# Kernel optimization log

Hardware: AMD Instinct MI355X
Metric: run time of the kernel (lower is better)

The kernel has to match this reference:

```python
import jax, jax.numpy as jnp
import numpy as np
from jax import lax

NUM_MASK_PARAMS = 67  # 66 weights (64 feat + 2 coord channels) + 1 bias
NUM_GEN_PARAMS = 134


def _coord_maps(h, w, dtype):
    yy = jnp.broadcast_to(jnp.linspace(-1.0, 1.0, h, dtype=dtype)[:, None], (h, w))
    xx = jnp.broadcast_to(jnp.linspace(-1.0, 1.0, w, dtype=dtype)[None, :], (h, w))
    return xx, yy


def _dynamic_head(x_cat, p):
    # x_cat: [66, H, W]; p: [num_ins, 67] -> [num_ins, H, W]
    w = p[:, :NUM_MASK_PARAMS - 1]
    b = p[:, NUM_MASK_PARAMS - 1]
    return jnp.einsum('ic,chw->ihw', w, x_cat) + b[:, None, None]


def setup_inputs() -> dict:
    key = jax.random.key(0)
    ks = jax.random.split(key, 10)
    C, HM, WM, HH, WH, MB, HID = 256, 272, 480, 136, 240, 64, 64
    rn = lambda k, s, sc=1.0: jax.random.normal(k, s, dtype=jnp.float32) * sc
    return {
        'out0': rn(ks[0], (1, C, HM, WM)),
        'out1': rn(ks[1], (1, C, HH, WH)),
        'hm_w': rn(ks[2], (1, C), 0.05),
        'hm_b': jnp.zeros((1,), jnp.float32),
        'params_w': rn(ks[3], (NUM_GEN_PARAMS, C), 0.05),
        'params_b': rn(ks[4], (NUM_GEN_PARAMS,), 0.05),
        'mb_w': rn(ks[5], (MB, C, 3, 3), 0.05),
        'mb_b': jnp.zeros((MB,), jnp.float32),
        'mlp_w1': rn(ks[6], (HM, HID), 0.05),
        'mlp_b1': jnp.zeros((HID,), jnp.float32),
        'mlp_w2': rn(ks[7], (HID, 2), 0.05),
        'mlp_b2': jnp.zeros((2,), jnp.float32),
        'num_ins': 4,
    }


def reference(out0, out1, hm_w, hm_b, params_w, params_b, mb_w, mb_b,
              mlp_w1, mlp_b1, mlp_w2, mlp_b2, num_ins):
    h_mask, w_mask = out0.shape[2], out0.shape[3]
    h_hm, w_hm = out1.shape[2], out1.shape[3]

    # ctnet head: 1x1 convs on the stride-16 feature
    hm = jnp.einsum('kc,bchw->bkhw', hm_w, out1) + hm_b[None, :, None, None]
    params = jnp.einsum('kc,bchw->bkhw', params_w, out1) + params_b[None, :, None, None]
    hm = jnp.clip(jax.nn.sigmoid(hm), 1e-4, 1.0 - 1e-4)  # [1,1,h_hm,w_hm]
    # [1,134,h,w] -> [h*w, 134]
    params_flat = jnp.transpose(params[0], (1, 2, 0)).reshape(-1, NUM_GEN_PARAMS)

    # 3x3 maxpool NMS (stride 1, pad 1), keep only local peaks
    hmax = lax.reduce_window(hm, -jnp.inf, lax.max, (1, 1, 3, 3), (1, 1, 1, 1),
                             [(0, 0), (0, 0), (1, 1), (1, 1)])
    keep = (hmax == hm).astype(hm.dtype)
    heat_nms = (hm * keep).reshape(-1)

    scores, inds = lax.top_k(heat_nms, num_ins)

    # mask branch: 3x3 conv + relu on the stride-8 feature
    mask_branch = lax.conv_general_dilated(out0, mb_w, (1, 1), 'SAME',
                                           dimension_numbers=('NCHW', 'OIHW', 'NCHW'))
    mask_branch = jax.nn.relu(mask_branch + mb_b[None, :, None, None])  # [1,64,H,W]

    xx, yy = _coord_maps(h_mask, w_mask, mask_branch.dtype)
    x_cat = jnp.concatenate([mask_branch[0], xx[None], yy[None]], axis=0)  # [66,H,W]

    gen_params = params_flat[inds]  # [num_ins, 134]
    masks0 = _dynamic_head(x_cat, gen_params[:, :NUM_MASK_PARAMS])   # [num_ins,H,W]
    regs0 = _dynamic_head(x_cat, gen_params[:, NUM_MASK_PARAMS:])    # [num_ins,H,W]

    # row-wise vertical-range MLP over h_mask
    feat_range = jnp.transpose(masks0, (0, 2, 1))  # [num_ins, w_mask, h_mask]
    h1 = jax.nn.relu(feat_range @ mlp_w1 + mlp_b1)
    feat_range = h1 @ mlp_w2 + mlp_b2  # [num_ins, w_mask, 2]

    return scores, inds, regs0, masks0, feat_range
```

## Files before the change

kernel.cpp:

```cpp
#include <hip/hip_runtime.h>
#include <math.h>
#include <limits.h>

#define C_IN 256
#define HM_H 136
#define HM_W 240
#define HM_N (HM_H * HM_W)
#define MB   64
#define MH   272
#define MW   480
#define MN   (MH * MW)
#define NP   134
#define NI   4
#define HID  64

#define REG_OFF   8
#define MASK_OFF  (8 + NI * MN)
#define FEAT_OFF  (8 + 2 * NI * MN)

#define WS_HM   0
#define WS_CV   HM_N
#define WS_CI   (HM_N + 512)
#define WS_GP   (2 * HM_N)
#define WS_WT_F 65824

typedef float  f32x4  __attribute__((ext_vector_type(4)));
typedef short  bf16x8 __attribute__((ext_vector_type(8)));
typedef unsigned int u32x4 __attribute__((ext_vector_type(4)));

__device__ __forceinline__ unsigned short f2bf(float f) {
  unsigned int u = __float_as_uint(f);
  u += 0x7FFFu + ((u >> 16) & 1u);
  return (unsigned short)(u >> 16);
}
__device__ __forceinline__ float b2f(unsigned short h) {
  return __uint_as_float(((unsigned int)h) << 16);
}
__device__ __forceinline__ unsigned cvtpk(float a, float b) {
  unsigned r;
  asm("v_cvt_pk_bf16_f32 %0, %1, %2" : "=v"(r) : "v"(a), "v"(b));
  return r;
}

__device__ __forceinline__ void glds16(const void* g, void* l) {
  __builtin_amdgcn_global_load_lds(
      (const __attribute__((address_space(1))) unsigned int*)g,
      (__attribute__((address_space(3))) unsigned int*)l, 16, 0, 0);
}

__global__ void k_prep(const float* __restrict__ mb_w, unsigned short* __restrict__ wt,
                       const float* __restrict__ out1, const float* __restrict__ hm_w,
                       const float* __restrict__ hm_b, float* __restrict__ ws_hm) {
  __shared__ float part[4][64];
  if (blockIdx.x < 576) {
    int idx = blockIdx.x * 256 + threadIdx.x;
    int j    = idx & 7;
    int lane = (idx >> 3) & 63;
    int nt   = (idx >> 9) & 3;
    int gt   = idx >> 11;
    int t    = gt % 9;
    int g    = gt / 9;
    int n = nt * 16 + (lane & 15);
    int c = g * 32 + (lane >> 4) * 8 + j;
    wt[idx] = f2bf(mb_w[(n * C_IN + c) * 9 + t]);
  } else {
    int b = blockIdx.x - 576, t = threadIdx.x;
    int cg = t >> 6, pl = t & 63;
    int p = b * 64 + pl;
    float s = 0.f;
    #pragma unroll 16
    for (int c = 0; c < 64; ++c)
      s += hm_w[cg * 64 + c] * out1[(cg * 64 + c) * HM_N + p];
    part[cg][pl] = s;
    __syncthreads();
    if (t < 64) {
      float tot = part[0][t] + part[1][t] + part[2][t] + part[3][t] + hm_b[0];
      float sig = 1.f / (1.f + expf(-tot));
      sig = fminf(fmaxf(sig, 1e-4f), 1.f - 1e-4f);
      ws_hm[b * 64 + t] = sig;
    }
  }
}

__device__ __forceinline__ bool better(float av, int ai, float bv, int bi) {
  return (av > bv) || (av == bv && ai < bi);
}

template<int NTHR>
__device__ void top4_tree(float* sv, int* si, int t) {
  for (int s = NTHR / 2; s >= 1; s >>= 1) {
    if (t < s) {
      float a[4], b[4]; int ai[4], bj[4];
      #pragma unroll
      for (int k = 0; k < 4; ++k) {
        a[k] = sv[t * 4 + k];        ai[k] = si[t * 4 + k];
        b[k] = sv[(t + s) * 4 + k];  bj[k] = si[(t + s) * 4 + k];
      }
      float ov[4]; int oi[4];
      int i = 0, j = 0;
      #pragma unroll
      for (int k = 0; k < 4; ++k) {
        if (better(a[i], ai[i], b[j], bj[j])) { ov[k] = a[i]; oi[k] = ai[i]; ++i; }
        else                                   { ov[k] = b[j]; oi[k] = bj[j]; ++j; }
      }
      #pragma unroll
      for (int k = 0; k < 4; ++k) { sv[t * 4 + k] = ov[k]; si[t * 4 + k] = oi[k]; }
    }
    __syncthreads();
  }
}

__global__ void k_nms_top(const float* __restrict__ ws_hm, float* __restrict__ candv,
                          int* __restrict__ candi) {
  __shared__ float sv[256 * 4];
  __shared__ int   si[256 * 4];
  int b = blockIdx.x, t = threadIdx.x;
  float v = -1.f; int idx = INT_MAX;
  if (t < 255) {
    int p = b * 255 + t;
    int y = p / HM_W, x = p - y * HM_W;
    float c = ws_hm[p], m = c;
    #pragma unroll
    for (int dy = -1; dy <= 1; ++dy)
      #pragma unroll
      for (int dx = -1; dx <= 1; ++dx) {
        int yy = y + dy, xx = x + dx;
        if (yy >= 0 && yy < HM_H && xx >= 0 && xx < HM_W)
          m = fmaxf(m, ws_hm[yy * HM_W + xx]);
      }
    v = (c == m) ? c : 0.f;
    idx = p;
  }
  sv[t * 4] = v; si[t * 4] = idx;
  #pragma unroll
  for (int k = 1; k < 4; ++k) { sv[t * 4 + k] = -1.f; si[t * 4 + k] = INT_MAX; }
  __syncthreads();
  top4_tree<256>(sv, si, t);
  if (t == 0) {
    #pragma unroll
    for (int k = 0; k < 4; ++k) { candv[b * 4 + k] = sv[k]; candi[b * 4 + k] = si[k]; }
  }
}

__global__ void k_gen(const float* __restrict__ candv, const int* __restrict__ candi,
                      const float* __restrict__ out1, const float* __restrict__ params_w,
                      const float* __restrict__ params_b, float* __restrict__ ws_gp,
                      float* __restrict__ d_out) {
  __shared__ float sv[128 * 4];
  __shared__ int   si[128 * 4];
  __shared__ float col[C_IN];
  __shared__ float part[NP];
  int t = threadIdx.x, i = blockIdx.x;
  if (t < 128) {
    #pragma unroll
    for (int k = 0; k < 4; ++k) { sv[t * 4 + k] = candv[t * 4 + k]; si[t * 4 + k] = candi[t * 4 + k]; }
  }
  __syncthreads();
  top4_tree<128>(sv, si, t);
  if (i == 0 && t < 4) {
    d_out[t]     = sv[t];
    d_out[4 + t] = (float)si[t];
  }
  int p = si[i];
  if (t < 256) col[t] = out1[t * HM_N + p];
  __syncthreads();
  int half = t >> 8, jj = t & 255;
  float s = 0.f;
  if (jj < NP) {
    s = half ? 0.f : params_b[jj];
    const float* pw = params_w + jj * C_IN + half * 128;
    const float* cl = col + half * 128;
    #pragma unroll 8
    for (int c = 0; c < 128; ++c) s += pw[c] * cl[c];
    if (half) part[jj] = s;
  }
  __syncthreads();
  if (!half && jj < NP) ws_gp[i * NP + jj] = s + part[jj];
}

#define SR   18
#define RP   36
#define BUFU (SR * RP * 32)
#define WBASE (2 * BUFU)
#define WBUFU 18432

#define PIPE_BARRIER() do {                                   \
    __builtin_amdgcn_sched_barrier(0);                        \
    asm volatile("s_waitcnt lgkmcnt(0)" ::: "memory");        \
    __builtin_amdgcn_s_barrier();                             \
    __builtin_amdgcn_sched_barrier(0);                        \
  } while (0)

#define STAGE_W_ALL(G)                                                    \
  if (wv == 7 && (G) < 8) {                                               \
    const char* wsrc = (const char*)wt + (G) * 36864 + lane * 16;         \
    char* wdst = (char*)smem + 82944 + ((G) & 1) * 36864;                 \
    _Pragma("unroll")                                                     \
    for (int i_ = 0; i_ < 36; ++i_)                                       \
      glds16(wsrc + i_ * 1024, wdst + i_ * 1024);                         \
  }

#define MFMA16(A, B, C) __builtin_amdgcn_mfma_f32_16x16x32_bf16(A, B, C, 0, 0, 0)

#define TAPS3(P) {                                                        \
    const unsigned short* wl = smem + WBASE + ((g) & 1) * WBUFU           \
                               + (P) * 6144 + lane * 8;                   \
    _Pragma("unroll")                                                     \
    for (int tt = 0; tt < 3; ++tt) {                                      \
      bf16x8 bb0 = *(const bf16x8*)(wl + tt * 2048);                      \
      bf16x8 bb1 = *(const bf16x8*)(wl + tt * 2048 + 512);                \
      bf16x8 bb2 = *(const bf16x8*)(wl + tt * 2048 + 1024);               \
      bf16x8 bb3 = *(const bf16x8*)(wl + tt * 2048 + 1536);               \
      unsigned pk = lrdp[(P) * 3 + tt];                                   \
      const unsigned short* c0 = cur + (pk & 0xFFFFu);                    \
      const unsigned short* c1 = cur + (pk >> 16);                        \
      bf16x8 a0 = *(const bf16x8*)c0;                                     \
      bf16x8 a1 = *(const bf16x8*)(c0 + 512);                             \
      bf16x8 a2 = *(const bf16x8*)c1;                                     \
      bf16x8 a3 = *(const bf16x8*)(c1 + 512);                             \
      acc[0][0] = MFMA16(a0, bb0, acc[0][0]);                             \
      acc[0][1] = MFMA16(a0, bb1, acc[0][1]);                             \
      acc[0][2] = MFMA16(a0, bb2, acc[0][2]);                             \
      acc[0][3] = MFMA16(a0, bb3, acc[0][3]);                             \
      acc[1][0] = MFMA16(a1, bb0, acc[1][0]);                             \
      acc[1][1] = MFMA16(a1, bb1, acc[1][1]);                             \
      acc[1][2] = MFMA16(a1, bb2, acc[1][2]);                             \
      acc[1][3] = MFMA16(a1, bb3, acc[1][3]);                             \
      acc[2][0] = MFMA16(a2, bb0, acc[2][0]);                             \
      acc[2][1] = MFMA16(a2, bb1, acc[2][1]);                             \
      acc[2][2] = MFMA16(a2, bb2, acc[2][2]);                             \
      acc[2][3] = MFMA16(a2, bb3, acc[2][3]);                             \
      acc[3][0] = MFMA16(a3, bb0, acc[3][0]);                             \
      acc[3][1] = MFMA16(a3, bb1, acc[3][1]);                             \
      acc[3][2] = MFMA16(a3, bb2, acc[3][2]);                             \
      acc[3][3] = MFMA16(a3, bb3, acc[3][3]);                             \
    } }

__device__ __forceinline__ void stage_store8(unsigned short* buf, const f32x4* dq,
                                             const int* lw, unsigned sm) {
  #pragma unroll
  for (int e = 0; e < 4; ++e) if ((sm >> e) & 1u) {
    u32x4 v;
    v[0] = cvtpk(dq[0][e], dq[1][e]);
    v[1] = cvtpk(dq[2][e], dq[3][e]);
    v[2] = cvtpk(dq[4][e], dq[5][e]);
    v[3] = cvtpk(dq[6][e], dq[7][e]);
    *(u32x4*)(buf + lw[e]) = v;
  }
}

__global__ __launch_bounds__(512, 2) void k_conv_mfma(
    const float* __restrict__ out0, const unsigned short* __restrict__ wt,
    const float* __restrict__ mb_b, const float* __restrict__ ws_gp,
    float* __restrict__ d_out) {
  __shared__ unsigned short smem[2 * BUFU + 2 * WBUFU];

  int tid  = threadIdx.x;
  int lane = tid & 63;
  int wv   = tid >> 6;
  int n15  = lane & 15;
  int kq   = lane >> 4;

  int orig = blockIdx.x;
  int xcd  = orig & 7, pos = orig >> 3;
  int wgid = (xcd < 7) ? (xcd * 32 + pos) : (224 + pos);
  int bx = wgid / 17, by = wgid - bx * 17;
  int gx0 = bx * 32, gy0 = by * 16;

  bool ustage = tid < 360;
  int u    = ustage ? tid : 0;
  int co8  = u / 180;
  int rem  = u - co8 * 180;
  int row  = rem / 10;
  int qx   = rem - row * 10;
  int iy   = gy0 + row - 1;
  int ixq  = gx0 + 4 * qx - 4;
  bool gvld = ustage && (iy >= 0) && (iy < MH) && (ixq >= 0) && (ixq + 3 < MW);
  int goffA = gvld ? (co8 * 8 * MN + iy * MW + ixq) : 0;
  int lwsA[4]; unsigned smask = 0;
  #pragma unroll
  for (int e = 0; e < 4; ++e) {
    int sx = 4 * qx - 3 + e;
    bool sv = ustage && (sx >= 0) && (sx < RP);
    int pixw = row * RP + (sv ? sx : 0);
    int w2 = (pixw ^ (pixw >> 2)) & 3;
    int q  = (pixw ^ row) & 1;
    lwsA[e] = (pixw >> 1) * 64 + ((co8 ^ w2) << 4) + q * 8;
    if (sv) smask |= (1u << e);
  }

  unsigned lrdp[9];
  #pragma unroll
  for (int t = 0; t < 9; ++t) {
    int ty = t / 3, tx = t - ty * 3;
    int sr0 = 2 * wv + ty;
    int pix0 = sr0 * RP + n15 + tx;
    int w20 = (pix0 ^ (pix0 >> 2)) & 3;
    int q0  = (pix0 ^ sr0) & 1;
    unsigned o0 = (pix0 >> 1) * 64 + ((kq ^ w20) << 4) + q0 * 8;
    int sr1 = sr0 + 1;
    int pix1 = sr1 * RP + n15 + tx;
    int w21 = (pix1 ^ (pix1 >> 2)) & 3;
    int q1  = (pix1 ^ sr1) & 1;
    unsigned o1 = (pix1 >> 1) * 64 + ((kq ^ w21) << 4) + q1 * 8;
    lrdp[t] = o0 | (o1 << 16);
  }

  f32x4 dqA[8], dqB[8];
  #pragma unroll
  for (int j = 0; j < 8; ++j) {
    dqA[j] = (f32x4){0.f, 0.f, 0.f, 0.f};
    dqB[j] = (f32x4){0.f, 0.f, 0.f, 0.f};
  }
  if (gvld) {
    const float* sp = out0 + goffA;
    #pragma unroll
    for (int j = 0; j < 8; ++j) dqA[j] = *(const f32x4*)(sp + j * MN);
  }
  stage_store8(smem, dqA, lwsA, smask);
  if (gvld) {
    const float* sp = out0 + goffA + 16 * MN;
    #pragma unroll
    for (int j = 0; j < 8; ++j) dqB[j] = *(const f32x4*)(sp + j * MN);
  }
  {
    int lwsB[4];
    #pragma unroll
    for (int e = 0; e < 4; ++e) lwsB[e] = lwsA[e] ^ 32;
    stage_store8(smem, dqB, lwsB, smask);
  }
  __builtin_amdgcn_sched_barrier(0);
  if (gvld) {
    const float* sp = out0 + 32 * MN + goffA;
    #pragma unroll
    for (int j = 0; j < 8; ++j) dqA[j] = *(const f32x4*)(sp + j * MN);
    const float* sq = out0 + 32 * MN + goffA + 16 * MN;
    #pragma unroll
    for (int j = 0; j < 8; ++j) dqB[j] = *(const f32x4*)(sq + j * MN);
  }
  __builtin_amdgcn_sched_barrier(0);
  STAGE_W_ALL(0);
  if (wv == 7) asm volatile("s_waitcnt vmcnt(0)" ::: "memory");
  PIPE_BARRIER();

  f32x4 acc[4][4];
  #pragma unroll
  for (int i = 0; i < 4; ++i)
    #pragma unroll
    for (int nt = 0; nt < 4; ++nt)
      acc[i][nt] = (f32x4){0.f, 0.f, 0.f, 0.f};

  #pragma unroll 1
  for (int g = 0; g < 8; ++g) {
    const unsigned short* cur = smem + (g & 1) * BUFU;
    unsigned short*       nxt = smem + ((g + 1) & 1) * BUFU;

    STAGE_W_ALL(g + 1);
    if (g < 7) {
      stage_store8(nxt, dqA, lwsA, smask);
      int lwsB[4];
      #pragma unroll
      for (int e = 0; e < 4; ++e) lwsB[e] = lwsA[e] ^ 32;
      stage_store8(nxt, dqB, lwsB, smask);
    }
    __builtin_amdgcn_sched_barrier(0);
    if (g < 6 && gvld) {
      const float* sp = out0 + (g + 2) * (32 * MN) + goffA;
      #pragma unroll
      for (int j = 0; j < 8; ++j) dqA[j] = *(const f32x4*)(sp + j * MN);
      const float* sq = out0 + (g + 2) * (32 * MN) + goffA + 16 * MN;
      #pragma unroll
      for (int j = 0; j < 8; ++j) dqB[j] = *(const f32x4*)(sq + j * MN);
    }
    __builtin_amdgcn_sched_barrier(0);

    TAPS3(0)
    TAPS3(1)
    TAPS3(2)

    if (wv == 7) asm volatile("s_waitcnt vmcnt(0)" ::: "memory");
    PIPE_BARRIER();
  }

  #define ES 66
  {
    float bias[4];
    #pragma unroll
    for (int nt = 0; nt < 4; ++nt) bias[nt] = mb_b[nt * 16 + n15];
    #pragma unroll
    for (int i = 0; i < 4; ++i) {
      int pbase = (2 * wv + (i >> 1)) * 32 + (i & 1) * 16;
      #pragma unroll
      for (int nt = 0; nt < 4; ++nt)
        #pragma unroll
        for (int reg = 0; reg < 4; ++reg) {
          float vv = fmaxf(acc[i][nt][reg] + bias[nt], 0.f);
          smem[(pbase + kq * 4 + reg) * ES + nt * 16 + n15] = f2bf(vv);
        }
    }
  }
  __syncthreads();

  int p = tid & 255, hh = tid >> 8;
  int ob = hh * 32;
  float* pf = (float*)smem + 16896;
  #pragma unroll 1
  for (int ps = 0; ps < 2; ++ps) {
    int pixel = ps * 256 + p;
    float mres[4] = {0.f, 0.f, 0.f, 0.f};
    float rres[4] = {0.f, 0.f, 0.f, 0.f};
    #pragma unroll 8
    for (int o = 0; o < 32; ++o) {
      float v = b2f(smem[pixel * ES + ob + o]);
      #pragma unroll
      for (int i = 0; i < 4; ++i) {
        mres[i] += ws_gp[i * NP + ob + o] * v;
        rres[i] += ws_gp[i * NP + 67 + ob + o] * v;
      }
    }
    if (hh) {
      #pragma unroll
      for (int i = 0; i < 4; ++i) { pf[p * 8 + i] = mres[i]; pf[p * 8 + 4 + i] = rres[i]; }
    }
    __syncthreads();
    if (!hh) {
      int r = pixel >> 5, xcol = pixel & 31;
      int gy = gy0 + r, gx = gx0 + xcol;
      float xc = -1.f + (2.f / 479.f) * (float)gx;
      float yc = -1.f + (2.f / 271.f) * (float)gy;
      int pix = gy * MW + gx;
      #pragma unroll
      for (int i = 0; i < 4; ++i) {
        const float* gp = ws_gp + i * NP;
        d_out[MASK_OFF + i * MN + pix] = mres[i] + pf[p * 8 + i]     + gp[66]  + gp[64]  * xc + gp[65]  * yc;
        d_out[REG_OFF  + i * MN + pix] = rres[i] + pf[p * 8 + 4 + i] + gp[133] + gp[131] * xc + gp[132] * yc;
      }
    }
    __syncthreads();
  }
}

__global__ void k_mlp(const float* __restrict__ masks0, const float* __restrict__ w1,
                      const float* __restrict__ b1, const float* __restrict__ w2,
                      const float* __restrict__ b2, float* __restrict__ d_out) {
  __shared__ float ms[MH];
  int blk = blockIdx.x;
  int i = blk / MW;
  int w = blk - i * MW;
  int k = threadIdx.x;
  const float* mcol = masks0 + i * MN + w;
  for (int h = k; h < MH; h += 64) ms[h] = mcol[h * MW];
  __syncthreads();
  float s = b1[k];
  #pragma unroll 8
  for (int h = 0; h < MH; ++h) s += ms[h] * w1[h * HID + k];
  s = fmaxf(s, 0.f);
  float o0 = s * w2[k * 2 + 0];
  float o1 = s * w2[k * 2 + 1];
  #pragma unroll
  for (int off = 32; off >= 1; off >>= 1) {
    o0 += __shfl_down(o0, off);
    o1 += __shfl_down(o1, off);
  }
  if (k == 0) {
    d_out[FEAT_OFF + blk * 2 + 0] = o0 + b2[0];
    d_out[FEAT_OFF + blk * 2 + 1] = o1 + b2[1];
  }
}

extern "C" void kernel_launch(void* const* d_in, const int* in_sizes, int n_in,
                              void* d_out, int out_size, void* d_ws, size_t ws_size,
                              hipStream_t stream) {
  const float* out0     = (const float*)d_in[0];
  const float* out1     = (const float*)d_in[1];
  const float* hm_w     = (const float*)d_in[2];
  const float* hm_b     = (const float*)d_in[3];
  const float* params_w = (const float*)d_in[4];
  const float* params_b = (const float*)d_in[5];
  const float* mb_w     = (const float*)d_in[6];
  const float* mb_b     = (const float*)d_in[7];
  const float* mlp_w1   = (const float*)d_in[8];
  const float* mlp_b1   = (const float*)d_in[9];
  const float* mlp_w2   = (const float*)d_in[10];
  const float* mlp_b2   = (const float*)d_in[11];

  float* ws      = (float*)d_ws;
  float* ws_hm   = ws + WS_HM;
  float* candv   = ws + WS_CV;
  int*   candi   = (int*)(ws + WS_CI);
  float* ws_gp   = ws + WS_GP;
  unsigned short* ws_wt = (unsigned short*)(ws + WS_WT_F);
  float* out     = (float*)d_out;

  k_prep<<<1086, 256, 0, stream>>>(mb_w, ws_wt, out1, hm_w, hm_b, ws_hm);
  k_nms_top<<<128, 256, 0, stream>>>(ws_hm, candv, candi);
  k_gen<<<NI, 512, 0, stream>>>(candv, candi, out1, params_w, params_b, ws_gp, out);
  k_conv_mfma<<<255, 512, 0, stream>>>(out0, ws_wt, mb_b, ws_gp, out);
  k_mlp<<<NI * MW, 64, 0, stream>>>(out + MASK_OFF, mlp_w1, mlp_b1, mlp_w2, mlp_b2, out);
}
```

Measured before the change: 295.9 us.

## Split conv K-loop into preload/MFMA phases interleaved with staging and priority boosts

Restructures the main 3x3 conv MFMA loop so that each kernel row's A and B fragments are loaded from LDS into registers first, then the 48 MFMAs run in a separate burst. Each burst is separated by a block barrier and raised wave priority (s_setprio). The global-load and LDS-staging work for the next channel group is placed between these bursts. The aim is to overlap memory traffic with matrix compute in a ping-pong style across waves. It adds three extra barriers per iteration and needs 96 extra VGPRs for the preloaded fragments, which may increase register pressure under launch bounds (512,2).

```diff
diff --git a/kernel.cpp b/kernel.cpp
--- a/kernel.cpp
+++ b/kernel.cpp
@@ -191,6 +191,13 @@
     __builtin_amdgcn_sched_barrier(0);                        \
   } while (0)
 
+#define PHASE_SYNC() do {                                     \
+    __builtin_amdgcn_sched_barrier(0);                        \
+    __builtin_amdgcn_s_barrier();                             \
+    asm volatile("s_waitcnt lgkmcnt(0)" ::: "memory");        \
+    __builtin_amdgcn_sched_barrier(0);                        \
+  } while (0)
+
 #define STAGE_W_ALL(G)                                                    \
   if (wv == 7 && (G) < 8) {                                               \
     const char* wsrc = (const char*)wt + (G) * 36864 + lane * 16;         \
@@ -202,39 +209,37 @@
 
 #define MFMA16(A, B, C) __builtin_amdgcn_mfma_f32_16x16x32_bf16(A, B, C, 0, 0, 0)
 
-#define TAPS3(P) {                                                        \
+#define PRELOAD(P)                                                        \
+  {                                                                       \
     const unsigned short* wl = smem + WBASE + ((g) & 1) * WBUFU           \
                                + (P) * 6144 + lane * 8;                   \
     _Pragma("unroll")                                                     \
     for (int tt = 0; tt < 3; ++tt) {                                      \
-      bf16x8 bb0 = *(const bf16x8*)(wl + tt * 2048);                      \
-      bf16x8 bb1 = *(const bf16x8*)(wl + tt * 2048 + 512);                \
-      bf16x8 bb2 = *(const bf16x8*)(wl + tt * 2048 + 1024);               \
-      bf16x8 bb3 = *(const bf16x8*)(wl + tt * 2048 + 1536);               \
+      RB[tt][0] = *(const bf16x8*)(wl + tt * 2048);                       \
+      RB[tt][1] = *(const bf16x8*)(wl + tt * 2048 + 512);                 \
+      RB[tt][2] = *(const bf16x8*)(wl + tt * 2048 + 1024);                \
+      RB[tt][3] = *(const bf16x8*)(wl + tt * 2048 + 1536);                \
       unsigned pk = lrdp[(P) * 3 + tt];                                   \
       const unsigned short* c0 = cur + (pk & 0xFFFFu);                    \
       const unsigned short* c1 = cur + (pk >> 16);                        \
-      bf16x8 a0 = *(const bf16x8*)c0;                                     \
-      bf16x8 a1 = *(const bf16x8*)(c0 + 512);                             \
-      bf16x8 a2 = *(const bf16x8*)c1;                                     \
-      bf16x8 a3 = *(const bf16x8*)(c1 + 512);                             \
-      acc[0][0] = MFMA16(a0, bb0, acc[0][0]);                             \
-      acc[0][1] = MFMA16(a0, bb1, acc[0][1]);                             \
-      acc[0][2] = MFMA16(a0, bb2, acc[0][2]);                             \
-      acc[0][3] = MFMA16(a0, bb3, acc[0][3]);                             \
-      acc[1][0] = MFMA16(a1, bb0, acc[1][0]);                             \
-      acc[1][1] = MFMA16(a1, bb1, acc[1][1]);                             \
-      acc[1][2] = MFMA16(a1, bb2, acc[1][2]);                             \
-      acc[1][3] = MFMA16(a1, bb3, acc[1][3]);                             \
-      acc[2][0] = MFMA16(a2, bb0, acc[2][0]);                             \
-      acc[2][1] = MFMA16(a2, bb1, acc[2][1]);                             \
-      acc[2][2] = MFMA16(a2, bb2, acc[2][2]);                             \
-      acc[2][3] = MFMA16(a2, bb3, acc[2][3]);                             \
-      acc[3][0] = MFMA16(a3, bb0, acc[3][0]);                             \
-      acc[3][1] = MFMA16(a3, bb1, acc[3][1]);                             \
-      acc[3][2] = MFMA16(a3, bb2, acc[3][2]);                             \
-      acc[3][3] = MFMA16(a3, bb3, acc[3][3]);                             \
-    } }
+      RA[tt][0] = *(const bf16x8*)c0;                                     \
+      RA[tt][1] = *(const bf16x8*)(c0 + 512);                             \
+      RA[tt][2] = *(const bf16x8*)c1;                                     \
+      RA[tt][3] = *(const bf16x8*)(c1 + 512);                             \
+    }                                                                     \
+  }
+
+#define MFMA48()                                                          \
+  _Pragma("unroll")                                                       \
+  for (int tt = 0; tt < 3; ++tt) {                                        \
+    _Pragma("unroll")                                                     \
+    for (int ii = 0; ii < 4; ++ii) {                                      \
+      acc[ii][0] = MFMA16(RA[tt][ii], RB[tt][0], acc[ii][0]);             \
+      acc[ii][1] = MFMA16(RA[tt][ii], RB[tt][1], acc[ii][1]);             \
+      acc[ii][2] = MFMA16(RA[tt][ii], RB[tt][2], acc[ii][2]);             \
+      acc[ii][3] = MFMA16(RA[tt][ii], RB[tt][3], acc[ii][3]);             \
+    }                                                                     \
+  }
 
 __device__ __forceinline__ void stage_store8(unsigned short* buf, const f32x4* dq,
                                              const int* lw, unsigned sm) {
@@ -354,8 +359,16 @@
   for (int g = 0; g < 8; ++g) {
     const unsigned short* cur = smem + (g & 1) * BUFU;
     unsigned short*       nxt = smem + ((g + 1) & 1) * BUFU;
-
+    bf16x8 RA[3][4], RB[3][4];
+
+    PRELOAD(0);
     STAGE_W_ALL(g + 1);
+    PHASE_SYNC();
+    __builtin_amdgcn_s_setprio(1);
+    MFMA48();
+    __builtin_amdgcn_s_setprio(0);
+
+    PRELOAD(1);
     if (g < 7) {
       stage_store8(nxt, dqA, lwsA, smask);
       int lwsB[4];
@@ -363,7 +376,12 @@
       for (int e = 0; e < 4; ++e) lwsB[e] = lwsA[e] ^ 32;
       stage_store8(nxt, dqB, lwsB, smask);
     }
-    __builtin_amdgcn_sched_barrier(0);
+    PHASE_SYNC();
+    __builtin_amdgcn_s_setprio(1);
+    MFMA48();
+    __builtin_amdgcn_s_setprio(0);
+
+    PRELOAD(2);
     if (g < 6 && gvld) {
       const float* sp = out0 + (g + 2) * (32 * MN) + goffA;
       #pragma unroll
@@ -372,11 +390,10 @@
       #pragma unroll
       for (int j = 0; j < 8; ++j) dqB[j] = *(const f32x4*)(sq + j * MN);
     }
-    __builtin_amdgcn_sched_barrier(0);
-
-    TAPS3(0)
-    TAPS3(1)
-    TAPS3(2)
+    PHASE_SYNC();
+    __builtin_amdgcn_s_setprio(1);
+    MFMA48();
+    __builtin_amdgcn_s_setprio(0);
 
     if (wv == 7) asm volatile("s_waitcnt vmcnt(0)" ::: "memory");
     PIPE_BARRIER();
```

After: 316.0 us. 1.07x slower.
